# Kernel tuning notes

Hardware: AMD Instinct MI355X
Metric: run time of the kernel (lower is better)

The kernel has to match this reference:

```python
import jax, jax.numpy as jnp
import numpy as np

U_A = 110.0  # upper bound of feature norm (init kwarg u_a)


def setup_inputs() -> dict:
    key = jax.random.key(0)
    k1, k2, k3, k4 = jax.random.split(key, 4)
    B, C = 256, 100000
    cos_theta = jax.random.normal(k1, (B, C), dtype=jnp.float32)
    cos_theta_m = jax.random.normal(k2, (B, C), dtype=jnp.float32)
    # feature norms in [l_a, u_a] = [10, 110]
    x_norm = 10.0 + 100.0 * jax.random.uniform(k3, (B,), dtype=jnp.float32)
    target = jax.random.randint(k4, (B,), 0, C, dtype=jnp.int32)
    return {"cos_theta": cos_theta, "cos_theta_m": cos_theta_m,
            "x_norm": x_norm, "target": target}


def reference(cos_theta, cos_theta_m, x_norm, target):
    B, C = cos_theta.shape
    # one-hot scatter: one_hot[i, target[i]] = 1 (world_size=1 -> full class dim)
    one_hot = jax.nn.one_hot(target, C, dtype=cos_theta.dtype)  # [B, C]
    # loss_G regularizer: g = x_norm / u_a^2 + 1 / x_norm
    loss_g = jnp.mean(x_norm / (U_A * U_A) + 1.0 / x_norm)
    # margin blend: use cos_theta_m at the target class, cos_theta elsewhere
    output = one_hot * cos_theta_m + (1.0 - one_hot) * cos_theta  # [B, C]
    # cross-entropy with stable log-softmax (distributed LSE collapses to this)
    logp = jax.nn.log_softmax(output, axis=-1)
    loss = -jnp.take_along_axis(logp, target[:, None], axis=-1)[:, 0]  # [B]
    return (loss.mean(), loss_g, one_hot)
```

## Files before the change

kernel.cpp:

```cpp
#include <hip/hip_runtime.h>


#define UA2_INV (1.0f / 12100.0f)

__global__ __launch_bounds__(1024) void magloss_row_kernel(
    const float* __restrict__ ct,
    const float* __restrict__ ctm,
    const int*   __restrict__ target,
    float*       __restrict__ onehot,
    float*       __restrict__ row_loss,
    int C)
{
    const int row = blockIdx.x;
    const size_t base = (size_t)row * (size_t)C;
    const int t = target[row];
    const float ctm_t = ctm[base + (size_t)t];

    const int nchunk = C >> 2;
    const int t4 = t >> 2;

    const float4* __restrict__ ct4 = (const float4*)(ct + base);
    float2* __restrict__ oh2 = (float2*)(onehot + base);

    float m = -1e30f;
    float s = 0.0f;

    for (int c = threadIdx.x; c < nchunk; c += blockDim.x) {
        float4 v = ct4[c];
        float2 o0 = make_float2(0.f, 0.f);
        float2 o1 = make_float2(0.f, 0.f);
        if (c == t4) {
            const int k = t & 3;
            if      (k == 0) { v.x = ctm_t; o0.x = 1.f; }
            else if (k == 1) { v.y = ctm_t; o0.y = 1.f; }
            else if (k == 2) { v.z = ctm_t; o1.x = 1.f; }
            else             { v.w = ctm_t; o1.y = 1.f; }
        }
        oh2[2 * c]     = o0;
        oh2[2 * c + 1] = o1;

        const float cmax = fmaxf(fmaxf(v.x, v.y), fmaxf(v.z, v.w));
        const float mn   = fmaxf(m, cmax);
        s = s * __expf(m - mn)
          + __expf(v.x - mn) + __expf(v.y - mn)
          + __expf(v.z - mn) + __expf(v.w - mn);
        m = mn;
    }

    for (int j = (nchunk << 2) + (int)threadIdx.x; j < C; j += blockDim.x) {
        const bool is_t = (j == t);
        const float v = is_t ? ctm_t : ct[base + (size_t)j];
        onehot[base + (size_t)j] = is_t ? 1.f : 0.f;
        const float mn = fmaxf(m, v);
        s = s * __expf(m - mn) + __expf(v - mn);
        m = mn;
    }

    #pragma unroll
    for (int off = 32; off; off >>= 1) {
        const float mo = __shfl_xor(m, off);
        const float so = __shfl_xor(s, off);
        const float M  = fmaxf(m, mo);
        s = s * __expf(m - M) + so * __expf(mo - M);
        m = M;
    }

    __shared__ float sm[16], ss[16];
    const int wave = threadIdx.x >> 6;
    const int lane = threadIdx.x & 63;
    if (lane == 0) { sm[wave] = m; ss[wave] = s; }
    __syncthreads();

    if (threadIdx.x == 0) {
        const int nwaves = blockDim.x >> 6;
        float M = sm[0], S = ss[0];
        for (int w = 1; w < nwaves; ++w) {
            const float mo = sm[w], so = ss[w];
            const float Mn = fmaxf(M, mo);
            S = S * __expf(M - Mn) + so * __expf(mo - Mn);
            M = Mn;
        }
        row_loss[row] = M + __logf(S) - ctm_t;
    }
}

__global__ __launch_bounds__(256) void magloss_finalize_kernel(
    const float* __restrict__ row_loss,
    const float* __restrict__ x_norm,
    float*       __restrict__ out,
    int B)
{
    const int i = threadIdx.x;
    float l = 0.f, g = 0.f;
    for (int j = i; j < B; j += blockDim.x) {
        l += row_loss[j];
        const float xn = x_norm[j];
        g += xn * UA2_INV + 1.0f / xn;
    }
    #pragma unroll
    for (int off = 32; off; off >>= 1) {
        l += __shfl_xor(l, off);
        g += __shfl_xor(g, off);
    }
    __shared__ float sl[4], sg[4];
    const int wave = i >> 6;
    const int lane = i & 63;
    if (lane == 0) { sl[wave] = l; sg[wave] = g; }
    __syncthreads();
    if (i == 0) {
        const int nw = blockDim.x >> 6;
        float L = 0.f, G = 0.f;
        for (int w = 0; w < nw; ++w) { L += sl[w]; G += sg[w]; }
        out[0] = L / (float)B;
        out[1] = G / (float)B;
    }
}

extern "C" void kernel_launch(void* const* d_in, const int* in_sizes, int n_in,
                              void* d_out, int out_size, void* d_ws, size_t ws_size,
                              hipStream_t stream) {
    const float* ct  = (const float*)d_in[0];
    const float* ctm = (const float*)d_in[1];
    const float* xn  = (const float*)d_in[2];
    const int*   tg  = (const int*)d_in[3];

    const int B = in_sizes[2];
    const int C = in_sizes[0] / B;

    float* out      = (float*)d_out;
    float* row_loss = (float*)d_ws;

    magloss_row_kernel<<<B, 1024, 0, stream>>>(ct, ctm, tg, out + 2, row_loss, C);
    magloss_finalize_kernel<<<1, 256, 0, stream>>>(row_loss, xn, out, B);
}
```

Before: 33.74 us.

## Split each row across eight blocks and merge partial log-sum-exp in finalize

The grid changes from one 1024-thread block per row to eight 256-thread blocks per row. Each block covers one column segment and writes a partial (max, sum) pair. The finalize kernel merges the eight partials per row and subtracts the target logit. The aim is more blocks than the MI355X has CUs, giving better load balance and latency hiding. The cost is a workspace write per block and more work in the single-block finalize.

```diff
diff --git a/kernel.cpp b/kernel.cpp
--- a/kernel.cpp
+++ b/kernel.cpp
@@ -2,21 +2,28 @@
 
 
 #define UA2_INV (1.0f / 12100.0f)
+#define SEG 8
+#define SEG_SHIFT 3
 
-__global__ __launch_bounds__(1024) void magloss_row_kernel(
+__global__ __launch_bounds__(256) void magloss_part_kernel(
     const float* __restrict__ ct,
     const float* __restrict__ ctm,
     const int*   __restrict__ target,
     float*       __restrict__ onehot,
-    float*       __restrict__ row_loss,
+    float*       __restrict__ part,
     int C)
 {
-    const int row = blockIdx.x;
+    const int bid = blockIdx.x;
+    const int row = bid >> SEG_SHIFT;
+    const int seg = bid & (SEG - 1);
     const size_t base = (size_t)row * (size_t)C;
     const int t = target[row];
     const float ctm_t = ctm[base + (size_t)t];
 
     const int nchunk = C >> 2;
+    const int cps = (nchunk + SEG - 1) >> SEG_SHIFT;
+    const int c0 = seg * cps;
+    const int c1 = min(c0 + cps, nchunk);
     const int t4 = t >> 2;
 
     const float4* __restrict__ ct4 = (const float4*)(ct + base);
@@ -25,7 +32,7 @@
     float m = -1e30f;
     float s = 0.0f;
 
-    for (int c = threadIdx.x; c < nchunk; c += blockDim.x) {
+    for (int c = c0 + (int)threadIdx.x; c < c1; c += 256) {
         float4 v = ct4[c];
         float2 o0 = make_float2(0.f, 0.f);
         float2 o1 = make_float2(0.f, 0.f);
@@ -47,13 +54,15 @@
         m = mn;
     }
 
-    for (int j = (nchunk << 2) + (int)threadIdx.x; j < C; j += blockDim.x) {
-        const bool is_t = (j == t);
-        const float v = is_t ? ctm_t : ct[base + (size_t)j];
-        onehot[base + (size_t)j] = is_t ? 1.f : 0.f;
-        const float mn = fmaxf(m, v);
-        s = s * __expf(m - mn) + __expf(v - mn);
-        m = mn;
+    if (seg == SEG - 1) {
+        for (int j = (nchunk << 2) + (int)threadIdx.x; j < C; j += 256) {
+            const bool is_t = (j == t);
+            const float v = is_t ? ctm_t : ct[base + (size_t)j];
+            onehot[base + (size_t)j] = is_t ? 1.f : 0.f;
+            const float mn = fmaxf(m, v);
+            s = s * __expf(m - mn) + __expf(v - mn);
+            m = mn;
+        }
     }
 
     #pragma unroll
@@ -65,36 +74,51 @@
         m = M;
     }
 
-    __shared__ float sm[16], ss[16];
+    __shared__ float sm[4], ss[4];
     const int wave = threadIdx.x >> 6;
     const int lane = threadIdx.x & 63;
     if (lane == 0) { sm[wave] = m; ss[wave] = s; }
     __syncthreads();
 
     if (threadIdx.x == 0) {
-        const int nwaves = blockDim.x >> 6;
         float M = sm[0], S = ss[0];
-        for (int w = 1; w < nwaves; ++w) {
+        #pragma unroll
+        for (int w = 1; w < 4; ++w) {
             const float mo = sm[w], so = ss[w];
             const float Mn = fmaxf(M, mo);
             S = S * __expf(M - Mn) + so * __expf(mo - Mn);
             M = Mn;
         }
-        row_loss[row] = M + __logf(S) - ctm_t;
+        part[2 * bid]     = M;
+        part[2 * bid + 1] = S;
     }
 }
 
 __global__ __launch_bounds__(256) void magloss_finalize_kernel(
-    const float* __restrict__ row_loss,
+    const float* __restrict__ part,
+    const float* __restrict__ ctm,
+    const int*   __restrict__ target,
     const float* __restrict__ x_norm,
     float*       __restrict__ out,
-    int B)
+    int B, int C)
 {
     const int i = threadIdx.x;
     float l = 0.f, g = 0.f;
-    for (int j = i; j < B; j += blockDim.x) {
-        l += row_loss[j];
-        const float xn = x_norm[j];
+    for (int r = i; r < B; r += 256) {
+        float M = part[2 * (r << SEG_SHIFT)];
+        float S = part[2 * (r << SEG_SHIFT) + 1];
+        #pragma unroll
+        for (int sgi = 1; sgi < SEG; ++sgi) {
+            const float mo = part[2 * ((r << SEG_SHIFT) + sgi)];
+            const float so = part[2 * ((r << SEG_SHIFT) + sgi) + 1];
+            const float Mn = fmaxf(M, mo);
+            S = S * __expf(M - Mn) + so * __expf(mo - Mn);
+            M = Mn;
+        }
+        const int t = target[r];
+        const float ctm_t = ctm[(size_t)r * (size_t)C + (size_t)t];
+        l += M + __logf(S) - ctm_t;
+        const float xn = x_norm[r];
         g += xn * UA2_INV + 1.0f / xn;
     }
     #pragma unroll
@@ -108,9 +132,9 @@
     if (lane == 0) { sl[wave] = l; sg[wave] = g; }
     __syncthreads();
     if (i == 0) {
-        const int nw = blockDim.x >> 6;
         float L = 0.f, G = 0.f;
-        for (int w = 0; w < nw; ++w) { L += sl[w]; G += sg[w]; }
+        #pragma unroll
+        for (int w = 0; w < 4; ++w) { L += sl[w]; G += sg[w]; }
         out[0] = L / (float)B;
         out[1] = G / (float)B;
     }
@@ -127,9 +151,9 @@
     const int B = in_sizes[2];
     const int C = in_sizes[0] / B;
 
-    float* out      = (float*)d_out;
-    float* row_loss = (float*)d_ws;
+    float* out  = (float*)d_out;
+    float* part = (float*)d_ws;
 
-    magloss_row_kernel<<<B, 1024, 0, stream>>>(ct, ctm, tg, out + 2, row_loss, C);
-    magloss_finalize_kernel<<<1, 256, 0, stream>>>(row_loss, xn, out, B);
+    magloss_part_kernel<<<B * SEG, 256, 0, stream>>>(ct, ctm, tg, out + 2, part, C);
+    magloss_finalize_kernel<<<1, 256, 0, stream>>>(part, ctm, tg, xn, out, B, C);
 }
```

New measurement: 34.34 us. No clear change (+1.8%).
